# Kernel tuning notes

Measured on AMD Instinct MI355X. Metric: run time of the kernel, lower is better.

## Reference

```python
import jax, jax.numpy as jnp
import numpy as np

B, S, DIN, DH, DOUT = 8, 2048, 512, 1024, 16


def setup_inputs() -> dict:
    key = jax.random.key(0)
    ks = jax.random.split(key, 7)
    x = jax.random.normal(ks[0], (B, S, DIN), dtype=jnp.float32)
    # MLP params (Linear stores W as [in, out] here; we apply x @ W + b)
    w1 = jax.random.normal(ks[1], (DIN, DH), dtype=jnp.float32) / np.sqrt(DIN)
    b1 = jnp.zeros((DH,), dtype=jnp.float32)
    w2 = jax.random.normal(ks[2], (DH, DH), dtype=jnp.float32) / np.sqrt(DH)
    b2 = jnp.zeros((DH,), dtype=jnp.float32)
    w3 = jax.random.normal(ks[3], (DH, DOUT), dtype=jnp.float32) / np.sqrt(DH)
    b3 = jnp.zeros((DOUT,), dtype=jnp.float32)
    # decay buffer: exact dyadics 1 - 2^-(c+3), matches init_kwargs list
    decay = 1.0 - 2.0 ** (-(jnp.arange(DOUT, dtype=jnp.float32) + 3.0))
    # D[i, t, c] = decay_c^(t - i) for t >= i else 0 (upper triangular per channel)
    idx = jnp.arange(S)
    exps = idx[None, :] - idx[:, None]            # [S, S], t - i
    mask = (exps >= 0).astype(jnp.float32)        # triu mask
    exps_c = jnp.maximum(exps, 0).astype(jnp.float32)
    D = mask[:, :, None] * (decay[None, None, :] ** exps_c[:, :, None])  # [S, S, DOUT]
    return {"input_temporal": x, "w1": w1, "b1": b1, "w2": w2, "b2": b2,
            "w3": w3, "b3": b3, "D": D}


def reference(input_temporal, w1, b1, w2, b2, w3, b3, D):
    # 3-layer MLP (dropout=0 -> identity in eval)
    h = jax.nn.relu(input_temporal @ w1 + b1)
    h = jax.nn.relu(h @ w2 + b2)
    o = h @ w3 + b3                               # [B, S, DOUT]
    # decay-weighted causal mixing: out[b,t,c] = sum_{i<=t} o[b,i,c] * decay_c^(t-i)
    # (equivalent to torch repeat+multiply+sum, without materializing [B,S,S,D])
    mixed = jnp.einsum('bic,itc->btc', o, D)
    # extra running cumsum as in the original forward
    return jnp.cumsum(mixed, axis=1)
```

## Files before the change

kernel.cpp:

```cpp
#include <hip/hip_runtime.h>

typedef unsigned int u32;
typedef unsigned short u16;
typedef float f32x4 __attribute__((ext_vector_type(4)));
typedef short bf16x8 __attribute__((ext_vector_type(8)));

__device__ __forceinline__ u16 f2bf(float f) {
  u32 u = __builtin_bit_cast(u32, f);
  u += 0x7FFFu + ((u >> 16) & 1u);
  return (u16)(u >> 16);
}
__device__ __forceinline__ void gload_lds16(const void* g, void* l) {
  __builtin_amdgcn_global_load_lds(
      (const __attribute__((address_space(1))) void*)g,
      (__attribute__((address_space(3))) void*)l, 16, 0, 0);
}
__device__ __forceinline__ u32 cvtpk_bf16(float lo, float hi) {
  u32 r;
  asm("v_cvt_pk_bf16_f32 %0, %1, %2" : "=v"(r) : "v"(lo), "v"(hi));
  return r;
}

__global__ __launch_bounds__(256) void prep_k(
    const float* __restrict__ w1, u16* __restrict__ w1t,
    const float* __restrict__ w2, u16* __restrict__ w2t,
    const float* __restrict__ w3, u16* __restrict__ w3t) {
  const int bid = blockIdx.x;
  const int tid = threadIdx.x;
  __shared__ float tile[32][33];
  const int z = bid >> 10, t = bid & 1023;
  const int bx = t & 31, by = t >> 5;
  const float* in; u16* out; int R, C;
  if (z == 0)      { in = w1; out = w1t; R = 512;  C = 1024; }
  else if (z == 1) { in = w2; out = w2t; R = 1024; C = 1024; }
  else             { in = w3; out = w3t; R = 1024; C = 16;   }
  int c0 = bx * 32, r0 = by * 32;
  if (c0 >= C || r0 >= R) return;
  int tx = tid & 31, ty = tid >> 5;
  #pragma unroll
  for (int j = 0; j < 4; j++) {
    int r = r0 + ty + j * 8, c = c0 + tx;
    if (r < R && c < C) tile[ty + j * 8][tx] = in[(size_t)r * C + c];
  }
  __syncthreads();
  #pragma unroll
  for (int j = 0; j < 4; j++) {
    int c = c0 + ty + j * 8, r = r0 + tx;
    if (r < R && c < C) out[(size_t)c * R + r] = f2bf(tile[tx][ty + j * 8]);
  }
}

__global__ __launch_bounds__(512, 2) void gemm1d_k(
    const float* __restrict__ X, const u16* __restrict__ Bt,
    const float* __restrict__ bias, u16* __restrict__ C,
    int M, int N, int K) {
  __shared__ __align__(16) char lds[3 * 49152];
  const int tid = threadIdx.x;
  const int rr = blockIdx.x;
  const int xcd = rr & 7, sid = rr >> 3;
  const int bm = (xcd << 3) | (sid >> 2);
  const int bnp = sid & 3;
  const int wave = tid >> 6, lane = tid & 63;
  const int wm = wave >> 1, wn = wave & 1;
  const int l15 = lane & 15, l4 = lane >> 4;
  const int NT = K >> 5;
  const size_t arow0 = (size_t)bm * 256, brow0 = (size_t)bnp * 256;

  f32x4 acc[2][4][4];
  #pragma unroll
  for (int h = 0; h < 2; h++)
    #pragma unroll
    for (int m = 0; m < 4; m++)
      #pragma unroll
      for (int n = 0; n < 4; n++) acc[h][m][n] = (f32x4){0.f, 0.f, 0.f, 0.f};

  auto stage = [&](int kt, int s) {
    char* sA = lds + s * 49152;
    char* sB = sA + 32768;
    #pragma unroll
    for (int j = 0; j < 4; j++) {
      int ch = tid + j * 512;
      int row = ch >> 3;
      int g = (ch & 7) ^ (row & 7);
      gload_lds16(X + (arow0 + row) * K + kt * 32 + g * 4, sA + ch * 16);
    }
    #pragma unroll
    for (int j = 0; j < 2; j++) {
      int ch = tid + j * 512;
      int row = ch >> 2;
      int col4 = (ch & 3) ^ (row & 3);
      gload_lds16(Bt + (brow0 + row) * K + kt * 32 + col4 * 8, sB + ch * 16);
    }
  };

  stage(0, 0);
  stage(1, 1);
  asm volatile("s_waitcnt vmcnt(6)" ::: "memory");
  __builtin_amdgcn_s_barrier();

  for (int t = 0; t < NT; t++) {
    const int s = t % 3;
    const char* sA = lds + s * 49152;
    const char* sB = sA + 32768;

    bf16x8 af[4];
    #pragma unroll
    for (int m = 0; m < 4; m++) {
      int r = wm * 64 + m * 16 + l15;
      f32x4 a0 = *(const f32x4*)(sA + r * 128 + ((((l4 << 1)) ^ (r & 7)) << 4));
      f32x4 a1 = *(const f32x4*)(sA + r * 128 + ((((l4 << 1) | 1) ^ (r & 7)) << 4));
      uint4 pk = {cvtpk_bf16(a0[0], a0[1]), cvtpk_bf16(a0[2], a0[3]),
                  cvtpk_bf16(a1[0], a1[1]), cvtpk_bf16(a1[2], a1[3])};
      af[m] = __builtin_bit_cast(bf16x8, pk);
    }
    bf16x8 b0[4];
    #pragma unroll
    for (int n = 0; n < 4; n++) {
      int r = wn * 64 + n * 16 + l15;
      b0[n] = *(const bf16x8*)(sB + r * 64 + ((l4 ^ (r & 3)) << 4));
    }
    if (t + 2 < NT) stage(t + 2, (t + 2) % 3);

    __builtin_amdgcn_s_barrier();
    asm volatile("s_waitcnt lgkmcnt(0)" ::: "memory");
    __builtin_amdgcn_sched_barrier(0);
    __builtin_amdgcn_s_setprio(1);
    #pragma unroll
    for (int m = 0; m < 4; m++)
      #pragma unroll
      for (int n = 0; n < 4; n++)
        acc[0][m][n] = __builtin_amdgcn_mfma_f32_16x16x32_bf16(
            af[m], b0[n], acc[0][m][n], 0, 0, 0);
    __builtin_amdgcn_s_setprio(0);

    bf16x8 b1[4];
    #pragma unroll
    for (int n = 0; n < 4; n++) {
      int r = 128 + wn * 64 + n * 16 + l15;
      b1[n] = *(const bf16x8*)(sB + r * 64 + ((l4 ^ (r & 3)) << 4));
    }
    __builtin_amdgcn_s_barrier();
    asm volatile("s_waitcnt lgkmcnt(0)" ::: "memory");
    __builtin_amdgcn_sched_barrier(0);
    __builtin_amdgcn_s_setprio(1);
    #pragma unroll
    for (int m = 0; m < 4; m++)
      #pragma unroll
      for (int n = 0; n < 4; n++)
        acc[1][m][n] = __builtin_amdgcn_mfma_f32_16x16x32_bf16(
            af[m], b1[n], acc[1][m][n], 0, 0, 0);
    __builtin_amdgcn_s_setprio(0);

    if (t + 1 < NT) {
      if (t + 2 < NT)
        asm volatile("s_waitcnt vmcnt(6)" ::: "memory");
      else
        asm volatile("s_waitcnt vmcnt(0)" ::: "memory");
      __builtin_amdgcn_s_barrier();
    }
  }

  #pragma unroll
  for (int h = 0; h < 2; h++) {
    int bn = bnp * 2 + h;
    #pragma unroll
    for (int n = 0; n < 4; n++) {
      int col = bn * 128 + wn * 64 + n * 16 + l15;
      float bv = bias[col];
      #pragma unroll
      for (int m = 0; m < 4; m++) {
        int row0 = bm * 256 + wm * 64 + m * 16 + l4 * 4;
        #pragma unroll
        for (int r = 0; r < 4; r++) {
          float v = acc[h][m][n][r] + bv;
          v = v > 0.f ? v : 0.f;
          C[(size_t)(row0 + r) * N + col] = f2bf(v);
        }
      }
    }
  }
}

__global__ __launch_bounds__(512, 2) void gemm2f_k(
    const u16* __restrict__ A, const u16* __restrict__ Bt,
    const float* __restrict__ bias, const u16* __restrict__ w3t,
    float* __restrict__ part, int M, int N, int K) {
  __shared__ __align__(16) char lds[131072];
  const int tid = threadIdx.x;
  const int rr = blockIdx.x;
  const int xcd = rr & 7, slot_id = rr >> 3;
  const int bm = (xcd << 3) | (slot_id >> 2);
  const int bn = slot_id & 3;
  const int wave = tid >> 6, lane = tid & 63;
  const int wm = wave >> 2, wn = wave & 3;
  const int l15 = lane & 15, l4 = lane >> 4;
  const int NT = K >> 5;
  const size_t arow0 = (size_t)bm * 256, brow0 = (size_t)bn * 256;

  f32x4 acc[4][8];
  #pragma unroll
  for (int p = 0; p < 4; p++)
    #pragma unroll
    for (int q = 0; q < 8; q++) acc[p][q] = (f32x4){0.f, 0.f, 0.f, 0.f};

  auto stage = [&](int kt, int s) {
    char* sA = lds + s * 32768;
    char* sB = sA + 16384;
    #pragma unroll
    for (int j = 0; j < 2; j++) {
      int ch = tid + j * 512;
      int row = ch >> 2;
      int col4 = (ch & 3) ^ (row & 3);
      gload_lds16(A + (arow0 + row) * K + kt * 32 + col4 * 8, sA + ch * 16);
    }
    #pragma unroll
    for (int j = 0; j < 2; j++) {
      int ch = tid + j * 512;
      int row = ch >> 2;
      int col4 = (ch & 3) ^ (row & 3);
      gload_lds16(Bt + (brow0 + row) * K + kt * 32 + col4 * 8, sB + ch * 16);
    }
  };

  stage(0, 0);
  stage(1, 1);
  stage(2, 2);
  asm volatile("s_waitcnt vmcnt(8)" ::: "memory");
  __builtin_amdgcn_s_barrier();

  for (int t = 0; t < NT; t++) {
    const int s = t & 3;
    const char* sA = lds + s * 32768;
    const char* sB = sA + 16384;

    bf16x8 bfr[4];
    #pragma unroll
    for (int n = 0; n < 4; n++) {
      int r = wn * 64 + n * 16 + l15;
      bfr[n] = *(const bf16x8*)(sB + r * 64 + ((l4 ^ (r & 3)) << 4));
    }
    bf16x8 af0[4];
    #pragma unroll
    for (int m = 0; m < 4; m++) {
      int r = wm * 128 + m * 16 + l15;
      af0[m] = *(const bf16x8*)(sA + r * 64 + ((l4 ^ (r & 3)) << 4));
    }
    if (t + 3 < NT) stage(t + 3, (t + 3) & 3);

    __builtin_amdgcn_s_barrier();
    asm volatile("s_waitcnt lgkmcnt(0)" ::: "memory");
    __builtin_amdgcn_sched_barrier(0);
    __builtin_amdgcn_s_setprio(1);
    #pragma unroll
    for (int p = 0; p < 4; p++)
      #pragma unroll
      for (int q = 0; q < 4; q++)
        acc[p][q] = __builtin_amdgcn_mfma_f32_16x16x32_bf16(
            bfr[p], af0[q], acc[p][q], 0, 0, 0);
    __builtin_amdgcn_s_setprio(0);

    bf16x8 af1[4];
    #pragma unroll
    for (int m = 0; m < 4; m++) {
      int r = wm * 128 + (m + 4) * 16 + l15;
      af1[m] = *(const bf16x8*)(sA + r * 64 + ((l4 ^ (r & 3)) << 4));
    }
    __builtin_amdgcn_s_barrier();
    asm volatile("s_waitcnt lgkmcnt(0)" ::: "memory");
    __builtin_amdgcn_sched_barrier(0);
    __builtin_amdgcn_s_setprio(1);
    #pragma unroll
    for (int p = 0; p < 4; p++)
      #pragma unroll
      for (int q = 0; q < 4; q++)
        acc[p][q + 4] = __builtin_amdgcn_mfma_f32_16x16x32_bf16(
            bfr[p], af1[q], acc[p][q + 4], 0, 0, 0);
    __builtin_amdgcn_s_setprio(0);

    if (t + 1 < NT) {
      if (t + 3 < NT)
        asm volatile("s_waitcnt vmcnt(8)" ::: "memory");
      else if (t + 2 < NT)
        asm volatile("s_waitcnt vmcnt(4)" ::: "memory");
      else
        asm volatile("s_waitcnt vmcnt(0)" ::: "memory");
      __builtin_amdgcn_s_barrier();
    }
  }

  __builtin_amdgcn_s_barrier();
  #pragma unroll
  for (int p = 0; p < 4; p++) {
    float4 bv = *(const float4*)(bias + wn * 64 + p * 16 + l4 * 4);
    int colb = (wn * 64 + p * 16 + l4 * 4) * 2;
    #pragma unroll
    for (int q = 0; q < 8; q++) {
      int hrow = wm * 128 + q * 16 + l15;
      float v0 = acc[p][q][0] + bv.x; v0 = v0 > 0.f ? v0 : 0.f;
      float v1 = acc[p][q][1] + bv.y; v1 = v1 > 0.f ? v1 : 0.f;
      float v2 = acc[p][q][2] + bv.z; v2 = v2 > 0.f ? v2 : 0.f;
      float v3 = acc[p][q][3] + bv.w; v3 = v3 > 0.f ? v3 : 0.f;
      uint2 pk;
      pk.x = (u32)f2bf(v0) | ((u32)f2bf(v1) << 16);
      pk.y = (u32)f2bf(v2) | ((u32)f2bf(v3) << 16);
      *(uint2*)(lds + hrow * 512 + (colb ^ ((hrow & 7) << 4))) = pk;
    }
  }
  __builtin_amdgcn_s_barrier();

  bf16x8 wf[8];
  {
    const u16* w3row = w3t + (size_t)l15 * 1024 + bn * 256 + l4 * 8;
    #pragma unroll
    for (int kk = 0; kk < 8; kk++)
      wf[kk] = *(const bf16x8*)(w3row + kk * 32);
  }
  #pragma unroll
  for (int g = 0; g < 2; g++) {
    int row0 = wave * 32 + g * 16;
    int row = row0 + l15;
    f32x4 oacc = (f32x4){0.f, 0.f, 0.f, 0.f};
    #pragma unroll
    for (int kk = 0; kk < 8; kk++) {
      bf16x8 hf = *(const bf16x8*)(lds + row * 512 +
                                   ((kk * 64 + l4 * 16) ^ ((row & 7) << 4)));
      oacc = __builtin_amdgcn_mfma_f32_16x16x32_bf16(hf, wf[kk], oacc,
                                                     0, 0, 0);
    }
    int grow = bm * 256 + row0 + l4 * 4;
    int b = grow >> 11, s = grow & 2047;
    float4 st = {oacc[0], oacc[1], oacc[2], oacc[3]};
    *(float4*)(part + ((size_t)bn * 128 + b * 16 + l15) * 2048 + s) = st;
  }
}

__global__ __launch_bounds__(64) void scan_k(
    const float* __restrict__ part, const float* __restrict__ b3,
    float* __restrict__ out) {
  const int chain = blockIdx.x;
  const int lane = threadIdx.x;
  const int b = chain >> 4, c = chain & 15;
  const float dinv = __builtin_bit_cast(float, (u32)((127 - (c + 3)) << 23));
  const float d = 1.f - dinv;
  const float b3c = b3[c];

  float o[32];
  #pragma unroll
  for (int i = 0; i < 8; i++) {
    float4 acc4 = {b3c, b3c, b3c, b3c};
    #pragma unroll
    for (int p = 0; p < 4; p++) {
      const float4* src = (const float4*)(part + (size_t)p * 262144 +
                                          (size_t)chain * 2048 + lane * 32);
      float4 v = src[i];
      acc4.x += v.x; acc4.y += v.y; acc4.z += v.z; acc4.w += v.w;
    }
    o[i * 4 + 0] = acc4.x; o[i * 4 + 1] = acc4.y;
    o[i * 4 + 2] = acc4.z; o[i * 4 + 3] = acc4.w;
  }

  float M = 0.f, A = 0.f, P = 1.f, S = 0.f;
  #pragma unroll
  for (int i = 0; i < 32; i++) {
    M = d * M + o[i];
    A += M;
    P *= d;
    S = d * S + d;
  }

  #pragma unroll
  for (int off = 1; off < 64; off <<= 1) {
    float Pp = __shfl_up(P, off, 64);
    float Mp = __shfl_up(M, off, 64);
    float Sp = __shfl_up(S, off, 64);
    float Ap = __shfl_up(A, off, 64);
    if (lane >= off) {
      float A2 = Ap + S * Mp + A;
      float S2 = Sp + S * Pp;
      float M2 = P * Mp + M;
      float P2 = Pp * P;
      A = A2; S = S2; M = M2; P = P2;
    }
  }
  float m0 = __shfl_up(M, 1, 64);
  float a0 = __shfl_up(A, 1, 64);
  if (lane == 0) { m0 = 0.f; a0 = 0.f; }

  float* dst = out + (size_t)b * 32768 + (size_t)(lane * 32) * 16 + c;
  float m = m0, a = a0;
  #pragma unroll
  for (int i = 0; i < 32; i++) {
    m = d * m + o[i];
    a += m;
    dst[i * 16] = a;
  }
}

extern "C" void kernel_launch(void* const* d_in, const int* in_sizes, int n_in,
                              void* d_out, int out_size, void* d_ws, size_t ws_size,
                              hipStream_t stream) {
  const float* x  = (const float*)d_in[0];
  const float* w1 = (const float*)d_in[1];
  const float* b1 = (const float*)d_in[2];
  const float* w2 = (const float*)d_in[3];
  const float* b2 = (const float*)d_in[4];
  const float* w3 = (const float*)d_in[5];
  const float* b3 = (const float*)d_in[6];
  float* out = (float*)d_out;

  char* ws = (char*)d_ws;
  size_t off = 0;
  u16* h1   = (u16*)(ws + off); off += (size_t)16384 * 1024 * 2;
  u16* w1t  = (u16*)(ws + off); off += (size_t)1024 * 512 * 2;
  u16* w2t  = (u16*)(ws + off); off += (size_t)1024 * 1024 * 2;
  u16* w3t  = (u16*)(ws + off); off += (size_t)16 * 1024 * 2;
  float* part = (float*)(ws + off); off += (size_t)4 * 128 * 2048 * 4;

  prep_k<<<3072, 256, 0, stream>>>(w1, w1t, w2, w2t, w3, w3t);
  gemm1d_k<<<256, 512, 0, stream>>>(x, w1t, b1, h1, 16384, 1024, 512);
  gemm2f_k<<<256, 512, 0, stream>>>(h1, w2t, b2, w3t, part,
                                    16384, 1024, 1024);
  scan_k<<<128, 64, 0, stream>>>(part, b3, out);
}
```

Baseline: 80.31 us.

## Stage fp32 A tile through registers and store bf16 to LDS in first GEMM

```diff
diff --git a/kernel.cpp b/kernel.cpp
--- a/kernel.cpp
+++ b/kernel.cpp
@@ -54,7 +54,7 @@
     const float* __restrict__ X, const u16* __restrict__ Bt,
     const float* __restrict__ bias, u16* __restrict__ C,
     int M, int N, int K) {
-  __shared__ __align__(16) char lds[3 * 49152];
+  __shared__ __align__(16) char lds[3 * 32768];
   const int tid = threadIdx.x;
   const int rr = blockIdx.x;
   const int xcd = rr & 7, sid = rr >> 3;
@@ -74,16 +74,8 @@
       #pragma unroll
       for (int n = 0; n < 4; n++) acc[h][m][n] = (f32x4){0.f, 0.f, 0.f, 0.f};
 
-  auto stage = [&](int kt, int s) {
-    char* sA = lds + s * 49152;
-    char* sB = sA + 32768;
-    #pragma unroll
-    for (int j = 0; j < 4; j++) {
-      int ch = tid + j * 512;
-      int row = ch >> 3;
-      int g = (ch & 7) ^ (row & 7);
-      gload_lds16(X + (arow0 + row) * K + kt * 32 + g * 4, sA + ch * 16);
-    }
+  auto stageB = [&](int kt, int s) {
+    char* sB = lds + s * 32768 + 16384;
     #pragma unroll
     for (int j = 0; j < 2; j++) {
       int ch = tid + j * 512;
@@ -92,26 +84,53 @@
       gload_lds16(Bt + (brow0 + row) * K + kt * 32 + col4 * 8, sB + ch * 16);
     }
   };
-
-  stage(0, 0);
-  stage(1, 1);
+  auto loadA = [&](int kt, float4 (&buf)[4]) {
+    #pragma unroll
+    for (int j = 0; j < 4; j++) {
+      int ch = tid + j * 512;
+      int row = ch >> 3;
+      int g = ch & 7;
+      buf[j] = *(const float4*)(X + (arow0 + row) * (size_t)K + kt * 32 + g * 4);
+    }
+  };
+  auto writeA = [&](float4 (&buf)[4], int s) {
+    char* sA = lds + s * 32768;
+    #pragma unroll
+    for (int j = 0; j < 4; j++) {
+      int ch = tid + j * 512;
+      int row = ch >> 3;
+      int g = ch & 7;
+      uint2 pk;
+      pk.x = cvtpk_bf16(buf[j].x, buf[j].y);
+      pk.y = cvtpk_bf16(buf[j].z, buf[j].w);
+      *(uint2*)(sA + row * 64 + ((((g >> 1) ^ (row & 3)) << 4) + (g & 1) * 8)) = pk;
+    }
+  };
+
+  float4 bufA[4], bufB[4];
+  loadA(0, bufA);
+  asm volatile("" ::: "memory");
+  stageB(0, 0);
+  asm volatile("" ::: "memory");
+  loadA(1, bufB);
+  asm volatile("" ::: "memory");
+  stageB(1, 1);
+  asm volatile("s_waitcnt vmcnt(8)" ::: "memory");
+  writeA(bufA, 0);
   asm volatile("s_waitcnt vmcnt(6)" ::: "memory");
+  asm volatile("s_waitcnt lgkmcnt(0)" ::: "memory");
   __builtin_amdgcn_s_barrier();
 
-  for (int t = 0; t < NT; t++) {
+  auto iter = [&](int t, float4 (&bufLoad)[4], float4 (&bufWrite)[4]) {
     const int s = t % 3;
-    const char* sA = lds + s * 49152;
-    const char* sB = sA + 32768;
+    const char* sA = lds + s * 32768;
+    const char* sB = sA + 16384;
 
     bf16x8 af[4];
     #pragma unroll
     for (int m = 0; m < 4; m++) {
       int r = wm * 64 + m * 16 + l15;
-      f32x4 a0 = *(const f32x4*)(sA + r * 128 + ((((l4 << 1)) ^ (r & 7)) << 4));
-      f32x4 a1 = *(const f32x4*)(sA + r * 128 + ((((l4 << 1) | 1) ^ (r & 7)) << 4));
-      uint4 pk = {cvtpk_bf16(a0[0], a0[1]), cvtpk_bf16(a0[2], a0[3]),
-                  cvtpk_bf16(a1[0], a1[1]), cvtpk_bf16(a1[2], a1[3])};
-      af[m] = __builtin_bit_cast(bf16x8, pk);
+      af[m] = *(const bf16x8*)(sA + r * 64 + ((l4 ^ (r & 3)) << 4));
     }
     bf16x8 b0[4];
     #pragma unroll
@@ -119,7 +138,11 @@
       int r = wn * 64 + n * 16 + l15;
       b0[n] = *(const bf16x8*)(sB + r * 64 + ((l4 ^ (r & 3)) << 4));
     }
-    if (t + 2 < NT) stage(t + 2, (t + 2) % 3);
+    if (t + 2 < NT) {
+      loadA(t + 2, bufLoad);
+      asm volatile("" ::: "memory");
+      stageB(t + 2, (t + 2) % 3);
+    }
 
     __builtin_amdgcn_s_barrier();
     asm volatile("s_waitcnt lgkmcnt(0)" ::: "memory");
@@ -133,6 +156,13 @@
             af[m], b0[n], acc[0][m][n], 0, 0, 0);
     __builtin_amdgcn_s_setprio(0);
 
+    if (t + 1 < NT) {
+      if (t + 2 < NT)
+        asm volatile("s_waitcnt vmcnt(8)" ::: "memory");
+      else
+        asm volatile("s_waitcnt vmcnt(2)" ::: "memory");
+      writeA(bufWrite, (t + 1) % 3);
+    }
     bf16x8 b1[4];
     #pragma unroll
     for (int n = 0; n < 4; n++) {
@@ -158,6 +188,11 @@
         asm volatile("s_waitcnt vmcnt(0)" ::: "memory");
       __builtin_amdgcn_s_barrier();
     }
+  };
+
+  for (int tt = 0; tt < NT; tt += 2) {
+    iter(tt, bufA, bufB);
+    iter(tt + 1, bufB, bufA);
   }
 
   #pragma unroll
```

Result: slower. 84.10 us (+4.7%).
